# Kernel optimization log

Measured on AMD Instinct MI355X. Metric: run time of the kernel, lower is better.

Reference implementation:

```python
import jax, jax.numpy as jnp
import numpy as np

N = 20000      # num nodes
E = 320000     # num edges (before self loops)
D = 512        # d_model
H = 4          # gnn_heads
C = 256        # gnn_hidden_dim (per-head out channels)
L = 4          # gnn_num_layers
B = 16         # number of graphs in batch
NEG_SLOPE = 0.2
LN_EPS = 1e-5


def setup_inputs() -> dict:
    key = jax.random.key(0)
    ks = jax.random.split(key, 10)
    s = 0.05
    return {
        "x": jax.random.normal(ks[0], (N, D), jnp.float32),
        "edge_index": jax.random.randint(ks[1], (2, E), 0, N, dtype=jnp.int32),
        "batch": jnp.sort(jax.random.randint(ks[2], (N,), 0, B, dtype=jnp.int32)),
        "W0": jax.random.normal(ks[3], (D, H * C), jnp.float32) * s,
        "W_rest": jax.random.normal(ks[4], (L - 1, H * C, H * C), jnp.float32) * s,
        "att_src": jax.random.normal(ks[5], (L, H, C), jnp.float32) * s,
        "att_dst": jax.random.normal(ks[6], (L, H, C), jnp.float32) * s,
        "conv_bias": jnp.zeros((L, H * C), jnp.float32),
        "proj_W": jax.random.normal(ks[7], (H * C, D), jnp.float32) * s,
        "proj_b": jnp.zeros((D,), jnp.float32),
        "ln_gamma": jnp.ones((D,), jnp.float32),
        "ln_beta": jnp.zeros((D,), jnp.float32),
    }


def _gat_layer(x, src, dst, W, a_src, a_dst, b):
    # x: [N, F_in] -> h: [N, H, C]
    h = (x @ W).reshape(N, H, C)
    alpha_src = jnp.einsum('nhc,hc->nh', h, a_src)   # [N, H]
    alpha_dst = jnp.einsum('nhc,hc->nh', h, a_dst)   # [N, H]
    e = jax.nn.leaky_relu(alpha_src[src] + alpha_dst[dst], NEG_SLOPE)  # [Etot, H]
    # per-destination softmax (every node has a self loop, so segments nonempty)
    m = jax.ops.segment_max(e, dst, num_segments=N)
    ex = jnp.exp(e - m[dst])
    denom = jax.ops.segment_sum(ex, dst, num_segments=N)
    alpha = ex / (denom[dst] + 1e-16)                # [Etot, H]
    out = jax.ops.segment_sum(alpha[:, :, None] * h[src], dst, num_segments=N)  # [N, H, C]
    return out.reshape(N, H * C) + b


def reference(x, edge_index, batch, W0, W_rest, att_src, att_dst, conv_bias,
              proj_W, proj_b, ln_gamma, ln_beta):
    # add self loops (PyG GATConv default)
    loop = jnp.arange(N, dtype=edge_index.dtype)
    src = jnp.concatenate([edge_index[0], loop])
    dst = jnp.concatenate([edge_index[1], loop])

    h = x
    for l in range(L):
        W = W0 if l == 0 else W_rest[l - 1]
        h = _gat_layer(h, src, dst, W, att_src[l], att_dst[l], conv_bias[l])
        h = jax.nn.relu(h)  # dropout: eval mode -> identity

    # global mean pool over nodes per graph
    sums = jax.ops.segment_sum(h, batch, num_segments=B)           # [B, H*C]
    counts = jax.ops.segment_sum(jnp.ones((N,), h.dtype), batch, num_segments=B)
    pooled = sums / jnp.maximum(counts, 1.0)[:, None]

    out = pooled @ proj_W + proj_b                                 # [B, D]
    mu = out.mean(-1, keepdims=True)
    var = ((out - mu) ** 2).mean(-1, keepdims=True)
    return (out - mu) / jnp.sqrt(var + LN_EPS) * ln_gamma + ln_beta
```

## Files before the change

kernel.cpp:

```cpp
#include <hip/hip_runtime.h>
#include <hip/hip_bf16.h>
#include <hip/hip_fp8.h>
#include <math.h>

#define Nn 20000
#define Ee 320000
#define Dd 512
#define Hh 4
#define Cc 256
#define Ll 4
#define Bb 16
#define HC 1024
#define ETOT (Ee + Nn)
#define NEG_SLOPE 0.2f
#define LN_EPS 1e-5f
#define NBLK ((Nn + 255) / 256)

typedef __attribute__((ext_vector_type(8))) __bf16 bf16x8;
typedef __attribute__((ext_vector_type(4))) __bf16 bf16x4;
typedef __attribute__((ext_vector_type(4))) float f32x4;
typedef __attribute__((ext_vector_type(2))) float f32x2;

__device__ __forceinline__ f32x4 fp8x4_to_f32(unsigned int v) {
#if __has_builtin(__builtin_amdgcn_cvt_pk_f32_fp8)
    f32x2 lo = __builtin_amdgcn_cvt_pk_f32_fp8((int)v, false);
    f32x2 hi = __builtin_amdgcn_cvt_pk_f32_fp8((int)v, true);
    f32x4 r; r[0] = lo[0]; r[1] = lo[1]; r[2] = hi[0]; r[3] = hi[1];
    return r;
#else
    f32x4 r;
    #pragma unroll
    for (int i = 0; i < 4; ++i) {
        __hip_fp8_e4m3 q; q.__x = (v >> (8 * i)) & 0xff;
        r[i] = (float)q;
    }
    return r;
#endif
}

__device__ __forceinline__ unsigned char f32_to_fp8(float f) {
    return __hip_fp8_e4m3(f).__x;
}


__device__ __forceinline__ void decode_edge(const int* ei, int e, int& s, int& d) {
    if (e < Ee) { s = ei[e]; d = ei[Ee + e]; }
    else        { s = e - Ee; d = e - Ee; }
}

__global__ void count_deg_kernel(const int* __restrict__ ei, int* __restrict__ deg) {
    int e = blockIdx.x * blockDim.x + threadIdx.x;
    if (e >= ETOT) return;
    int s, d; decode_edge(ei, e, s, d);
    atomicAdd(&deg[d], 1);
}

__global__ void scan1_kernel(const int* __restrict__ deg, int* __restrict__ tmp,
                             int* __restrict__ bsum) {
    __shared__ int sd[256];
    int tid = threadIdx.x;
    int i = blockIdx.x * 256 + tid;
    sd[tid] = (i < Nn) ? deg[i] : 0;
    __syncthreads();
    for (int off = 1; off < 256; off <<= 1) {
        int t = (tid >= off) ? sd[tid - off] : 0;
        __syncthreads();
        sd[tid] += t;
        __syncthreads();
    }
    if (i < Nn) tmp[i] = sd[tid];
    if (tid == 255) bsum[blockIdx.x] = sd[255];
}

__global__ void scan2_kernel(int* __restrict__ bsum) {
    __shared__ int sd[256];
    int tid = threadIdx.x;
    sd[tid] = (tid < NBLK) ? bsum[tid] : 0;
    __syncthreads();
    for (int off = 1; off < 256; off <<= 1) {
        int t = (tid >= off) ? sd[tid - off] : 0;
        __syncthreads();
        sd[tid] += t;
        __syncthreads();
    }
    if (tid < NBLK) bsum[tid] = sd[tid];
}

__global__ void scan3_kernel(const int* __restrict__ tmp, const int* __restrict__ bsum,
                             const int* __restrict__ deg,
                             int* __restrict__ row_ptr, int* __restrict__ cursor) {
    int i = blockIdx.x * 256 + threadIdx.x;
    if (i >= Nn) return;
    int boff = (blockIdx.x == 0) ? 0 : bsum[blockIdx.x - 1];
    int incl = tmp[i] + boff;
    row_ptr[i + 1] = incl;
    cursor[i] = incl - deg[i];
    if (i == 0) row_ptr[0] = 0;
}

__global__ void scatter_kernel(const int* __restrict__ ei, int* __restrict__ cursor,
                               int* __restrict__ csr_src) {
    int e = blockIdx.x * blockDim.x + threadIdx.x;
    if (e >= ETOT) return;
    int s, d; decode_edge(ei, e, s, d);
    int pos = atomicAdd(&cursor[d], 1);
    csr_src[pos] = s;
}


__global__ void cast_kernel(const float* __restrict__ in, __bf16* __restrict__ out, int n4) {
    int i = blockIdx.x * blockDim.x + threadIdx.x;
    if (i >= n4) return;
    f32x4 v = ((const f32x4*)in)[i];
    bf16x4 o;
    #pragma unroll
    for (int k = 0; k < 4; ++k) o[k] = (__bf16)v[k];
    ((bf16x4*)out)[i] = o;
}

__global__ void transpose_cast_kernel(const float* __restrict__ W, __bf16* __restrict__ WT,
                                      int K, int N) {
    __shared__ float tile[32][33];
    W  += (size_t)blockIdx.z * K * N;
    WT += (size_t)blockIdx.z * K * N;
    int n0 = blockIdx.x * 32, k0 = blockIdx.y * 32;
    for (int i = threadIdx.y; i < 32; i += 8)
        tile[i][threadIdx.x] = W[(size_t)(k0 + i) * N + n0 + threadIdx.x];
    __syncthreads();
    for (int i = threadIdx.y; i < 32; i += 8)
        WT[(size_t)(n0 + i) * K + k0 + threadIdx.x] = (__bf16)tile[threadIdx.x][i];
}


__device__ __forceinline__ void async16(const __bf16* g, __bf16* l) {
    __builtin_amdgcn_global_load_lds((const __attribute__((address_space(1))) void*)g,
                                     (__attribute__((address_space(3))) void*)l,
                                     16, 0, 0);
}

__global__ __launch_bounds__(256) void mfma_gemm_kernel(
    const __bf16* __restrict__ A,
    const __bf16* __restrict__ BT,
    unsigned char* __restrict__ C8,
    const float* __restrict__ att_s,
    const float* __restrict__ att_d,
    float* __restrict__ aprt_s,
    float* __restrict__ aprt_d,
    int M, int K)
{
    int lin = blockIdx.y * 8 + blockIdx.x;
    int rblk = (lin >> 6) * 8 + (lin & 7);
    int cblk = (lin >> 3) & 7;
    int rowBase = rblk * 128, colBase = cblk * 128;
    if (rowBase >= M) return;

    __shared__ __bf16 As[2][128 * 32];
    __shared__ __bf16 Bs[2][128 * 32];
    int tid = threadIdx.x;
    int wave = tid >> 6, lane = tid & 63;
    int m16 = lane & 15, quad = lane >> 4;
    int waveRow = (wave >> 1) * 64, waveCol = (wave & 1) * 64;

    f32x4 acc[4][4] = {};

    int srow = wave * 32 + (lane >> 2);
    int gch0 = (lane & 3) ^ ((srow >> 1) & 3);
    int gch1 = (lane & 3) ^ (((srow + 16) >> 1) & 3);
    int gr0 = rowBase + srow;       if (gr0 >= M) gr0 = M - 1;
    int gr1 = rowBase + srow + 16;  if (gr1 >= M) gr1 = M - 1;
    int ldsOff = srow * 32 + (lane & 3) * 8;

    for (int k0 = 0; k0 < K; k0 += 64) {
        #pragma unroll
        for (int p = 0; p < 2; ++p) {
            int kp = k0 + p * 32;
            async16(A + (size_t)gr0 * K + kp + gch0 * 8, &As[p][ldsOff]);
            async16(A + (size_t)gr1 * K + kp + gch1 * 8, &As[p][ldsOff + 16 * 32]);
            async16(BT + (size_t)(colBase + srow) * K + kp + gch0 * 8, &Bs[p][ldsOff]);
            async16(BT + (size_t)(colBase + srow + 16) * K + kp + gch1 * 8, &Bs[p][ldsOff + 16 * 32]);
        }
        __syncthreads();
        #pragma unroll
        for (int p = 0; p < 2; ++p) {
            bf16x8 af[4], bfr[4];
            #pragma unroll
            for (int i = 0; i < 4; ++i) {
                int row = waveRow + i * 16 + m16;
                af[i] = *(const bf16x8*)&As[p][row * 32 + (quad ^ ((row >> 1) & 3)) * 8];
                int col = waveCol + i * 16 + m16;
                bfr[i] = *(const bf16x8*)&Bs[p][col * 32 + (quad ^ ((col >> 1) & 3)) * 8];
            }
            #pragma unroll
            for (int i = 0; i < 4; ++i)
                #pragma unroll
                for (int j = 0; j < 4; ++j)
                    acc[i][j] = __builtin_amdgcn_mfma_f32_16x16x32_bf16(af[i], bfr[j], acc[i][j], 0, 0, 0);
        }
        __syncthreads();
    }

    int cbase = colBase + waveCol;
    int head = cbase >> 8;
    int part = (cblk & 1) * 2 + (wave & 1);
    float as4[4], ad4[4];
    #pragma unroll
    for (int j = 0; j < 4; ++j) {
        int off = (cbase + j * 16 + m16) & 255;
        as4[j] = att_s[head * 256 + off];
        ad4[j] = att_d[head * 256 + off];
    }

    #pragma unroll
    for (int i = 0; i < 4; ++i) {
        int r0 = rowBase + waveRow + i * 16 + quad * 4;
        #pragma unroll
        for (int r = 0; r < 4; ++r) {
            int row = r0 + r;
            float ps = 0.f, pd = 0.f;
            #pragma unroll
            for (int j = 0; j < 4; ++j) {
                float h = acc[i][j][r];
                ps += h * as4[j];
                pd += h * ad4[j];
                if (row < M)
                    C8[(size_t)row * HC + colBase + waveCol + j * 16 + m16] = f32_to_fp8(h);
            }
            #pragma unroll
            for (int off = 1; off < 16; off <<= 1) {
                ps += __shfl_xor(ps, off);
                pd += __shfl_xor(pd, off);
            }
            if (m16 == 0 && row < M) {
                aprt_s[((size_t)part * M + row) * 4 + head] = ps;
                aprt_d[((size_t)part * M + row) * 4 + head] = pd;
            }
        }
    }
}


__global__ void alpha_sum_kernel(const float* __restrict__ aprt_s,
                                 const float* __restrict__ aprt_d,
                                 float* __restrict__ asrc, float* __restrict__ adst) {
    int n = blockIdx.x * 256 + threadIdx.x;
    if (n >= Nn) return;
    f32x4 s = {0.f, 0.f, 0.f, 0.f}, d = {0.f, 0.f, 0.f, 0.f};
    #pragma unroll
    for (int p = 0; p < 4; ++p) {
        f32x4 vs = ((const f32x4*)aprt_s)[(size_t)p * Nn + n];
        f32x4 vd = ((const f32x4*)aprt_d)[(size_t)p * Nn + n];
        #pragma unroll
        for (int k = 0; k < 4; ++k) { s[k] += vs[k]; d[k] += vd[k]; }
    }
    ((f32x4*)asrc)[n] = s;
    ((f32x4*)adst)[n] = d;
}


__global__ __launch_bounds__(256) void ew_kernel(const float* __restrict__ asrc,
                                                 const float* __restrict__ adst,
                                                 const int* __restrict__ row_ptr,
                                                 const int* __restrict__ csr_src,
                                                 float* __restrict__ ewT,
                                                 float* __restrict__ dinv) {
    int w = threadIdx.x >> 6, lane = threadIdx.x & 63;
    int n = blockIdx.x * 4 + w;
    if (n >= Nn) return;
    int start = row_ptr[n], end = row_ptr[n + 1];
    f32x4 ad = ((const f32x4*)adst)[n];
    f32x4 d = {0.f, 0.f, 0.f, 0.f};
    for (int e = start + lane; e < end; e += 64) {
        int s = csr_src[e];
        f32x4 as = ((const f32x4*)asrc)[s];
        #pragma unroll
        for (int k = 0; k < 4; ++k) {
            float z = as[k] + ad[k];
            z = (z > 0.f) ? z : NEG_SLOPE * z;
            float ex = __expf(z);
            ewT[(size_t)k * ETOT + e] = ex;
            d[k] += ex;
        }
    }
    #pragma unroll
    for (int off = 32; off > 0; off >>= 1) {
        #pragma unroll
        for (int k = 0; k < 4; ++k) d[k] += __shfl_down(d[k], off);
    }
    if (lane == 0) {
        f32x4 iv;
        #pragma unroll
        for (int k = 0; k < 4; ++k) iv[k] = 1.f / (d[k] + 1e-16f);
        ((f32x4*)dinv)[n] = iv;
    }
}


__global__ __launch_bounds__(256) void agg_slice_kernel(
    const unsigned char* __restrict__ h8,
    const float* __restrict__ ewT,
    const float* __restrict__ dinv,
    const int* __restrict__ row_ptr,
    const int* __restrict__ csr_src,
    const float* __restrict__ bias_l,
    __bf16* __restrict__ outb)
{
    int slice = blockIdx.x;
    int head = slice >> 1;
    int tid = threadIdx.x;
    int nslot = tid >> 4;
    int ch = tid & 15;
    int n = blockIdx.y * 16 + nslot;

    __shared__ int   csr_sh[512];
    __shared__ float ew_sh[512];
    __shared__ int   rp_sh[17];

    if (tid < 17) rp_sh[tid] = row_ptr[blockIdx.y * 16 + tid];
    __syncthreads();
    int blk_lo = rp_sh[0], blk_hi = rp_sh[16];
    int start = rp_sh[nslot], end = rp_sh[nslot + 1];

    const unsigned char* hs = h8 + slice * 128 + ch * 8;
    const float* ewh = ewT + (size_t)head * ETOT;
    float acc[8] = {};

    for (int c0 = blk_lo; c0 < blk_hi; c0 += 512) {
        int c1 = min(c0 + 512, blk_hi);
        int cnt = c1 - c0;
        for (int i = tid; i < cnt; i += 256) {
            csr_sh[i] = csr_src[c0 + i];
            ew_sh[i]  = ewh[c0 + i];
        }
        __syncthreads();
        int lo = max(start, c0), hi = min(end, c1);
        int e = lo;
        for (; e + 1 < hi; e += 2) {
            int s0 = csr_sh[e - c0], s1 = csr_sh[e + 1 - c0];
            float w0 = ew_sh[e - c0], w1 = ew_sh[e + 1 - c0];
            uint2 u0 = *(const uint2*)(hs + (size_t)s0 * HC);
            uint2 u1 = *(const uint2*)(hs + (size_t)s1 * HC);
            f32x4 a0 = fp8x4_to_f32(u0.x), b0 = fp8x4_to_f32(u0.y);
            f32x4 a1 = fp8x4_to_f32(u1.x), b1 = fp8x4_to_f32(u1.y);
            #pragma unroll
            for (int k = 0; k < 4; ++k) {
                acc[k]     += w0 * a0[k];
                acc[k + 4] += w0 * b0[k];
                acc[k]     += w1 * a1[k];
                acc[k + 4] += w1 * b1[k];
            }
        }
        if (e < hi) {
            int s0 = csr_sh[e - c0];
            float w0 = ew_sh[e - c0];
            uint2 u0 = *(const uint2*)(hs + (size_t)s0 * HC);
            f32x4 a0 = fp8x4_to_f32(u0.x), b0 = fp8x4_to_f32(u0.y);
            #pragma unroll
            for (int k = 0; k < 4; ++k) {
                acc[k]     += w0 * a0[k];
                acc[k + 4] += w0 * b0[k];
            }
        }
        __syncthreads();
    }

    float inv = dinv[n * 4 + head];
    bf16x8 o;
    #pragma unroll
    for (int k = 0; k < 8; ++k)
        o[k] = (__bf16)fmaxf(acc[k] * inv + bias_l[slice * 128 + ch * 8 + k], 0.f);
    *(bf16x8*)(outb + (size_t)n * HC + slice * 128 + ch * 8) = o;
}


__device__ __forceinline__ int lower_bound_batch(const int* __restrict__ batch, int val) {
    int lo = 0, hi = Nn;
    while (lo < hi) { int mid = (lo + hi) >> 1; if (batch[mid] < val) lo = mid + 1; else hi = mid; }
    return lo;
}

__global__ void pool_kernel(const __bf16* __restrict__ h2b, const int* __restrict__ batch,
                            float* __restrict__ pooledP) {
    int b = blockIdx.x, part = blockIdx.y;
    int tid = threadIdx.x;
    int start = lower_bound_batch(batch, b);
    int end   = lower_bound_batch(batch, b + 1);
    int len = end - start;
    int chunk = (len + 7) / 8;
    int s0 = start + part * chunk;
    int s1 = min(s0 + chunk, end);
    float acc[4] = {0.f, 0.f, 0.f, 0.f};
    for (int n = s0; n < s1; ++n) {
        bf16x4 v = ((const bf16x4*)(h2b + (size_t)n * HC))[tid];
        #pragma unroll
        for (int k = 0; k < 4; ++k) acc[k] += (float)v[k];
    }
    #pragma unroll
    for (int k = 0; k < 4; ++k)
        pooledP[((size_t)part * Bb + b) * HC + tid * 4 + k] = acc[k];
}


__global__ __launch_bounds__(512) void proj_partial_kernel(const float* __restrict__ pooledP,
                                                           const int* __restrict__ batch,
                                                           const float* __restrict__ projW,
                                                           float* __restrict__ projP) {
    int b = blockIdx.x, part = blockIdx.y;
    int d = threadIdx.x;
    __shared__ float psum[HC];
    int start = lower_bound_batch(batch, b);
    int end   = lower_bound_batch(batch, b + 1);
    float inv = 1.0f / fmaxf((float)(end - start), 1.0f);
    for (int k = d; k < HC; k += 512) {
        float s = 0.f;
        #pragma unroll
        for (int p = 0; p < 8; ++p) s += pooledP[((size_t)p * Bb + b) * HC + k];
        psum[k] = s * inv;
    }
    __syncthreads();
    float acc = 0.f;
    int k0 = part * 128;
    for (int k = k0; k < k0 + 128; ++k)
        acc += psum[k] * projW[(size_t)k * Dd + d];
    projP[((size_t)part * Bb + b) * Dd + d] = acc;
}

__global__ __launch_bounds__(512) void ln_kernel(const float* __restrict__ projP,
                                                 const float* __restrict__ projb,
                                                 const float* __restrict__ gamma,
                                                 const float* __restrict__ beta,
                                                 float* __restrict__ out) {
    int b = blockIdx.x;
    int d = threadIdx.x;
    __shared__ float red[512];
    float o = projb[d];
    #pragma unroll
    for (int p = 0; p < 8; ++p) o += projP[((size_t)p * Bb + b) * Dd + d];
    red[d] = o;
    __syncthreads();
    for (int off = 256; off > 0; off >>= 1) {
        if (d < off) red[d] += red[d + off];
        __syncthreads();
    }
    float mu = red[0] / (float)Dd;
    __syncthreads();
    float df = o - mu;
    red[d] = df * df;
    __syncthreads();
    for (int off = 256; off > 0; off >>= 1) {
        if (d < off) red[d] += red[d + off];
        __syncthreads();
    }
    float var = red[0] / (float)Dd;
    out[b * Dd + d] = df / sqrtf(var + LN_EPS) * gamma[d] + beta[d];
}


extern "C" void kernel_launch(void* const* d_in, const int* in_sizes, int n_in,
                              void* d_out, int out_size, void* d_ws, size_t ws_size,
                              hipStream_t stream) {
    const float* x         = (const float*)d_in[0];
    const int*   ei        = (const int*)d_in[1];
    const int*   batch     = (const int*)d_in[2];
    const float* W0        = (const float*)d_in[3];
    const float* W_rest    = (const float*)d_in[4];
    const float* att_src   = (const float*)d_in[5];
    const float* att_dst   = (const float*)d_in[6];
    const float* conv_bias = (const float*)d_in[7];
    const float* proj_W    = (const float*)d_in[8];
    const float* proj_b    = (const float*)d_in[9];
    const float* ln_gamma  = (const float*)d_in[10];
    const float* ln_beta   = (const float*)d_in[11];
    float* out = (float*)d_out;

    char* ws = (char*)d_ws;
    size_t off = 0;
    auto alloc = [&](size_t bytes) {
        void* p = ws + off;
        off = (off + bytes + 255) & ~(size_t)255;
        return p;
    };
    unsigned char* h8 = (unsigned char*)alloc((size_t)Nn * HC);
    __bf16* h2b     = (__bf16*)alloc((size_t)Nn * HC * 2);
    __bf16* xb      = (__bf16*)alloc((size_t)Nn * Dd * 2);
    __bf16* W0T     = (__bf16*)alloc((size_t)HC * Dd * 2);
    __bf16* WrT     = (__bf16*)alloc((size_t)3 * HC * HC * 2);
    float*  aprt_s  = (float*)alloc((size_t)4 * Nn * Hh * 4);
    float*  aprt_d  = (float*)alloc((size_t)4 * Nn * Hh * 4);
    float*  asrc    = (float*)alloc((size_t)Nn * Hh * 4);
    float*  adst    = (float*)alloc((size_t)Nn * Hh * 4);
    float*  ewT     = (float*)alloc((size_t)Hh * ETOT * 4);
    float*  dinv    = (float*)alloc((size_t)Nn * Hh * 4);
    int*    deg     = (int*)alloc((size_t)Nn * 4);
    int*    tmp     = (int*)alloc((size_t)Nn * 4);
    int*    bsum    = (int*)alloc((size_t)256 * 4);
    int*    row_ptr = (int*)alloc((size_t)(Nn + 1) * 4);
    int*    cursor  = (int*)alloc((size_t)Nn * 4);
    int*    csr_src = (int*)alloc((size_t)ETOT * 4);
    float*  pooledP = (float*)alloc((size_t)8 * Bb * HC * 4);
    float*  projP   = (float*)alloc((size_t)8 * Bb * Dd * 4);
    (void)ws_size; (void)in_sizes; (void)n_in; (void)out_size;

    hipMemsetAsync(deg, 0, (size_t)Nn * 4, stream);
    count_deg_kernel<<<(ETOT + 255) / 256, 256, 0, stream>>>(ei, deg);
    scan1_kernel<<<NBLK, 256, 0, stream>>>(deg, tmp, bsum);
    scan2_kernel<<<1, 256, 0, stream>>>(bsum);
    scan3_kernel<<<NBLK, 256, 0, stream>>>(tmp, bsum, deg, row_ptr, cursor);
    scatter_kernel<<<(ETOT + 255) / 256, 256, 0, stream>>>(ei, cursor, csr_src);

    cast_kernel<<<(Nn * Dd / 4 + 255) / 256, 256, 0, stream>>>(x, xb, Nn * Dd / 4);
    transpose_cast_kernel<<<dim3(HC / 32, Dd / 32, 1), dim3(32, 8), 0, stream>>>(W0, W0T, Dd, HC);
    transpose_cast_kernel<<<dim3(HC / 32, HC / 32, 3), dim3(32, 8), 0, stream>>>(W_rest, WrT, HC, HC);

    dim3 gemm_grid(8, 160);
    for (int l = 0; l < Ll; ++l) {
        const __bf16* Afeat = (l == 0) ? xb : h2b;
        int K = (l == 0) ? Dd : HC;
        const __bf16* BT = (l == 0) ? W0T : (WrT + (size_t)(l - 1) * HC * HC);
        mfma_gemm_kernel<<<gemm_grid, 256, 0, stream>>>(
            Afeat, BT, h8, att_src + l * HC, att_dst + l * HC, aprt_s, aprt_d, Nn, K);
        alpha_sum_kernel<<<NBLK, 256, 0, stream>>>(aprt_s, aprt_d, asrc, adst);
        ew_kernel<<<(Nn + 3) / 4, 256, 0, stream>>>(asrc, adst, row_ptr, csr_src, ewT, dinv);
        agg_slice_kernel<<<dim3(8, Nn / 16), 256, 0, stream>>>(
            h8, ewT, dinv, row_ptr, csr_src, conv_bias + l * HC, h2b);
    }

    pool_kernel<<<dim3(Bb, 8), 256, 0, stream>>>(h2b, batch, pooledP);
    proj_partial_kernel<<<dim3(Bb, 8), 512, 0, stream>>>(pooledP, batch, proj_W, projP);
    ln_kernel<<<Bb, 512, 0, stream>>>(projP, proj_b, ln_gamma, ln_beta, out);
}
```

Before: 650.3 us.

## Double-buffer GEMM with 128x256 tiles, 512 threads and prefetch overlap

The GEMM moves from 128x128 tiles with 4 waves to 128x256 tiles with 8 waves, doubling the LDS buffers. The next k-tile is staged asynchronously while the MFMAs on the current one run, using explicit vmcnt waits, raw barriers and setprio around the MFMA block. The goal is to hide global-load latency and raise B-tile reuse. In exchange, LDS use per block rises to 96KB, which lowers occupancy, and the hand-tuned waitcnt logic is fragile.

```diff
diff --git a/kernel.cpp b/kernel.cpp
--- a/kernel.cpp
+++ b/kernel.cpp
@@ -138,7 +138,39 @@
                                      16, 0, 0);
 }
 
-__global__ __launch_bounds__(256) void mfma_gemm_kernel(
+#define GEMM_PHASE(BUF, KP, DO_STAGE, KT_NEXT, VM_LAST)                                   \
+  {                                                                                       \
+    bf16x8 af[4], bv[4];                                                                  \
+    _Pragma("unroll")                                                                     \
+    for (int i = 0; i < 4; ++i) {                                                         \
+        int row = waveRow + i * 16 + m16;                                                 \
+        af[i] = *(const bf16x8*)&As[BUF][KP][row * 32 + ((quad ^ ((row >> 1) & 3)) << 3)];\
+        int col = waveCol + i * 16 + m16;                                                 \
+        bv[i] = *(const bf16x8*)&Bs[BUF][KP][col * 32 + ((quad ^ ((col >> 1) & 3)) << 3)];\
+    }                                                                                     \
+    if (DO_STAGE) {                                                                       \
+        int kk = (KT_NEXT) * 64 + (KP) * 32;                                              \
+        async16(A  + (size_t)gra  * K + kk + (gca << 3), &As[(BUF) ^ 1][KP][ldsA]);       \
+        async16(BT + (size_t)grb  * K + kk + (gcb << 3), &Bs[(BUF) ^ 1][KP][ldsB]);       \
+        async16(BT + (size_t)grb2 * K + kk + (gcb << 3), &Bs[(BUF) ^ 1][KP][ldsB2]);      \
+    }                                                                                     \
+    if (VM_LAST) { asm volatile("s_waitcnt vmcnt(0)" ::: "memory"); }                     \
+    else         { asm volatile("s_waitcnt vmcnt(3)" ::: "memory"); }                     \
+    __builtin_amdgcn_s_barrier();                                                         \
+    asm volatile("s_waitcnt lgkmcnt(0)" ::: "memory");                                    \
+    __builtin_amdgcn_sched_barrier(0);                                                    \
+    __builtin_amdgcn_s_setprio(1);                                                        \
+    _Pragma("unroll")                                                                     \
+    for (int i = 0; i < 4; ++i)                                                           \
+        _Pragma("unroll")                                                                 \
+        for (int j = 0; j < 4; ++j)                                                       \
+            acc[i][j] = __builtin_amdgcn_mfma_f32_16x16x32_bf16(af[i], bv[j],             \
+                                                                acc[i][j], 0, 0, 0);      \
+    __builtin_amdgcn_s_setprio(0);                                                        \
+    __builtin_amdgcn_s_barrier();                                                         \
+  }
+
+__global__ __launch_bounds__(512) void mfma_gemm_kernel(
     const __bf16* __restrict__ A,
     const __bf16* __restrict__ BT,
     unsigned char* __restrict__ C8,
@@ -148,60 +180,54 @@
     float* __restrict__ aprt_d,
     int M, int K)
 {
-    int lin = blockIdx.y * 8 + blockIdx.x;
-    int rblk = (lin >> 6) * 8 + (lin & 7);
-    int cblk = (lin >> 3) & 7;
-    int rowBase = rblk * 128, colBase = cblk * 128;
+    int lin = blockIdx.y * 4 + blockIdx.x;
+    int rblk = (lin >> 5) * 8 + (lin & 7);
+    int cblk = (lin >> 3) & 3;
+    int rowBase = rblk * 128, colBase = cblk * 256;
     if (rowBase >= M) return;
 
-    __shared__ __bf16 As[2][128 * 32];
-    __shared__ __bf16 Bs[2][128 * 32];
+    __shared__ __bf16 As[2][2][128 * 32];
+    __shared__ __bf16 Bs[2][2][256 * 32];
     int tid = threadIdx.x;
     int wave = tid >> 6, lane = tid & 63;
     int m16 = lane & 15, quad = lane >> 4;
-    int waveRow = (wave >> 1) * 64, waveCol = (wave & 1) * 64;
+    int wm = wave >> 2, wn = wave & 3;
+    int waveRow = wm * 64, waveCol = wn * 64;
 
     f32x4 acc[4][4] = {};
 
-    int srow = wave * 32 + (lane >> 2);
-    int gch0 = (lane & 3) ^ ((srow >> 1) & 3);
-    int gch1 = (lane & 3) ^ (((srow + 16) >> 1) & 3);
-    int gr0 = rowBase + srow;       if (gr0 >= M) gr0 = M - 1;
-    int gr1 = rowBase + srow + 16;  if (gr1 >= M) gr1 = M - 1;
-    int ldsOff = srow * 32 + (lane & 3) * 8;
-
-    for (int k0 = 0; k0 < K; k0 += 64) {
-        #pragma unroll
-        for (int p = 0; p < 2; ++p) {
-            int kp = k0 + p * 32;
-            async16(A + (size_t)gr0 * K + kp + gch0 * 8, &As[p][ldsOff]);
-            async16(A + (size_t)gr1 * K + kp + gch1 * 8, &As[p][ldsOff + 16 * 32]);
-            async16(BT + (size_t)(colBase + srow) * K + kp + gch0 * 8, &Bs[p][ldsOff]);
-            async16(BT + (size_t)(colBase + srow + 16) * K + kp + gch1 * 8, &Bs[p][ldsOff + 16 * 32]);
-        }
-        __syncthreads();
-        #pragma unroll
-        for (int p = 0; p < 2; ++p) {
-            bf16x8 af[4], bfr[4];
-            #pragma unroll
-            for (int i = 0; i < 4; ++i) {
-                int row = waveRow + i * 16 + m16;
-                af[i] = *(const bf16x8*)&As[p][row * 32 + (quad ^ ((row >> 1) & 3)) * 8];
-                int col = waveCol + i * 16 + m16;
-                bfr[i] = *(const bf16x8*)&Bs[p][col * 32 + (quad ^ ((col >> 1) & 3)) * 8];
-            }
-            #pragma unroll
-            for (int i = 0; i < 4; ++i)
-                #pragma unroll
-                for (int j = 0; j < 4; ++j)
-                    acc[i][j] = __builtin_amdgcn_mfma_f32_16x16x32_bf16(af[i], bfr[j], acc[i][j], 0, 0, 0);
-        }
-        __syncthreads();
+    int srow = tid >> 2;
+    int chk  = tid & 3;
+    int gca  = chk ^ ((srow >> 1) & 3);
+    int gcb  = gca;
+    int gra  = rowBase + srow;  if (gra >= M) gra = M - 1;
+    int grb  = colBase + srow;
+    int grb2 = colBase + srow + 128;
+    int ldsA  = srow * 32 + chk * 8;
+    int ldsB  = srow * 32 + chk * 8;
+    int ldsB2 = ldsB + 128 * 32;
+
+    #pragma unroll
+    for (int kp = 0; kp < 2; ++kp) {
+        int kk = kp * 32;
+        async16(A  + (size_t)gra  * K + kk + (gca << 3), &As[0][kp][ldsA]);
+        async16(BT + (size_t)grb  * K + kk + (gcb << 3), &Bs[0][kp][ldsB]);
+        async16(BT + (size_t)grb2 * K + kk + (gcb << 3), &Bs[0][kp][ldsB2]);
+    }
+    asm volatile("s_waitcnt vmcnt(3)" ::: "memory");
+    __builtin_amdgcn_s_barrier();
+
+    int NT = K >> 6;
+    for (int kt = 0; kt < NT; ++kt) {
+        int buf = kt & 1;
+        bool more = (kt + 1 < NT);
+        GEMM_PHASE(buf, 0, more, kt + 1, !more);
+        GEMM_PHASE(buf, 1, more, kt + 1, false);
     }
 
     int cbase = colBase + waveCol;
     int head = cbase >> 8;
-    int part = (cblk & 1) * 2 + (wave & 1);
+    int part = wn;
     float as4[4], ad4[4];
     #pragma unroll
     for (int j = 0; j < 4; ++j) {
@@ -223,12 +249,12 @@
                 ps += h * as4[j];
                 pd += h * ad4[j];
                 if (row < M)
-                    C8[(size_t)row * HC + colBase + waveCol + j * 16 + m16] = f32_to_fp8(h);
+                    C8[(size_t)row * HC + cbase + j * 16 + m16] = f32_to_fp8(h);
             }
             #pragma unroll
-            for (int off = 1; off < 16; off <<= 1) {
-                ps += __shfl_xor(ps, off);
-                pd += __shfl_xor(pd, off);
+            for (int off2 = 1; off2 < 16; off2 <<= 1) {
+                ps += __shfl_xor(ps, off2);
+                pd += __shfl_xor(pd, off2);
             }
             if (m16 == 0 && row < M) {
                 aprt_s[((size_t)part * M + row) * 4 + head] = ps;
@@ -511,12 +537,12 @@
     transpose_cast_kernel<<<dim3(HC / 32, Dd / 32, 1), dim3(32, 8), 0, stream>>>(W0, W0T, Dd, HC);
     transpose_cast_kernel<<<dim3(HC / 32, HC / 32, 3), dim3(32, 8), 0, stream>>>(W_rest, WrT, HC, HC);
 
-    dim3 gemm_grid(8, 160);
+    dim3 gemm_grid(4, 160);
     for (int l = 0; l < Ll; ++l) {
         const __bf16* Afeat = (l == 0) ? xb : h2b;
         int K = (l == 0) ? Dd : HC;
         const __bf16* BT = (l == 0) ? W0T : (WrT + (size_t)(l - 1) * HC * HC);
-        mfma_gemm_kernel<<<gemm_grid, 256, 0, stream>>>(
+        mfma_gemm_kernel<<<gemm_grid, 512, 0, stream>>>(
             Afeat, BT, h8, att_src + l * HC, att_dst + l * HC, aprt_s, aprt_d, Nn, K);
         alpha_sum_kernel<<<NBLK, 256, 0, stream>>>(aprt_s, aprt_d, asrc, adst);
         ew_kernel<<<(Nn + 3) / 4, 256, 0, stream>>>(asrc, adst, row_ptr, csr_src, ewT, dinv);
```

Measured after the change: 722.0 us. 1.11x slower.

## Narrow per-node thread groups in edge-weight and aggregation kernels

Applied to the files above, without the earlier changes.

The edge-weight kernel now gives each node 16 lanes instead of a full 64-lane wavefront, since the average degree is about 17, and reduces with xor shuffles. The aggregation kernel now covers 32 nodes per block with 8 threads per node, each loading 16 fp8 bytes per gathered row instead of 8. Edge source and weight are packed into one int2 shared array with a larger staging chunk, and the 2-way edge unroll is dropped. The goal is fewer idle lanes and fewer, wider gather loads, at the cost of more registers per thread and less unrolling for memory-level parallelism.

```diff
diff --git a/kernel.cpp b/kernel.cpp
--- a/kernel.cpp
+++ b/kernel.cpp
@@ -263,13 +263,13 @@
                                                  const int* __restrict__ csr_src,
                                                  float* __restrict__ ewT,
                                                  float* __restrict__ dinv) {
-    int w = threadIdx.x >> 6, lane = threadIdx.x & 63;
-    int n = blockIdx.x * 4 + w;
+    int grp = threadIdx.x >> 4, lane16 = threadIdx.x & 15;
+    int n = blockIdx.x * 16 + grp;
     if (n >= Nn) return;
     int start = row_ptr[n], end = row_ptr[n + 1];
     f32x4 ad = ((const f32x4*)adst)[n];
     f32x4 d = {0.f, 0.f, 0.f, 0.f};
-    for (int e = start + lane; e < end; e += 64) {
+    for (int e = start + lane16; e < end; e += 16) {
         int s = csr_src[e];
         f32x4 as = ((const f32x4*)asrc)[s];
         #pragma unroll
@@ -282,11 +282,11 @@
         }
     }
     #pragma unroll
-    for (int off = 32; off > 0; off >>= 1) {
-        #pragma unroll
-        for (int k = 0; k < 4; ++k) d[k] += __shfl_down(d[k], off);
-    }
-    if (lane == 0) {
+    for (int off = 8; off > 0; off >>= 1) {
+        #pragma unroll
+        for (int k = 0; k < 4; ++k) d[k] += __shfl_xor(d[k], off);
+    }
+    if (lane16 == 0) {
         f32x4 iv;
         #pragma unroll
         for (int k = 0; k < 4; ++k) iv[k] = 1.f / (d[k] + 1e-16f);
@@ -307,68 +307,59 @@
     int slice = blockIdx.x;
     int head = slice >> 1;
     int tid = threadIdx.x;
-    int nslot = tid >> 4;
-    int ch = tid & 15;
-    int n = blockIdx.y * 16 + nslot;
-
-    __shared__ int   csr_sh[512];
-    __shared__ float ew_sh[512];
-    __shared__ int   rp_sh[17];
-
-    if (tid < 17) rp_sh[tid] = row_ptr[blockIdx.y * 16 + tid];
-    __syncthreads();
-    int blk_lo = rp_sh[0], blk_hi = rp_sh[16];
+    int nslot = tid >> 3;
+    int ch = tid & 7;
+    int n = blockIdx.y * 32 + nslot;
+
+    __shared__ int2 ce_sh[1024];
+    __shared__ int  rp_sh[33];
+
+    if (tid < 33) rp_sh[tid] = row_ptr[blockIdx.y * 32 + tid];
+    __syncthreads();
+    int blk_lo = rp_sh[0], blk_hi = rp_sh[32];
     int start = rp_sh[nslot], end = rp_sh[nslot + 1];
 
-    const unsigned char* hs = h8 + slice * 128 + ch * 8;
+    const unsigned char* hs = h8 + slice * 128 + ch * 16;
     const float* ewh = ewT + (size_t)head * ETOT;
-    float acc[8] = {};
-
-    for (int c0 = blk_lo; c0 < blk_hi; c0 += 512) {
-        int c1 = min(c0 + 512, blk_hi);
+    float acc[16] = {};
+
+    for (int c0 = blk_lo; c0 < blk_hi; c0 += 1024) {
+        int c1 = min(c0 + 1024, blk_hi);
         int cnt = c1 - c0;
         for (int i = tid; i < cnt; i += 256) {
-            csr_sh[i] = csr_src[c0 + i];
-            ew_sh[i]  = ewh[c0 + i];
+            int2 v;
+            v.x = csr_src[c0 + i];
+            v.y = __float_as_int(ewh[c0 + i]);
+            ce_sh[i] = v;
         }
         __syncthreads();
         int lo = max(start, c0), hi = min(end, c1);
-        int e = lo;
-        for (; e + 1 < hi; e += 2) {
-            int s0 = csr_sh[e - c0], s1 = csr_sh[e + 1 - c0];
-            float w0 = ew_sh[e - c0], w1 = ew_sh[e + 1 - c0];
-            uint2 u0 = *(const uint2*)(hs + (size_t)s0 * HC);
-            uint2 u1 = *(const uint2*)(hs + (size_t)s1 * HC);
-            f32x4 a0 = fp8x4_to_f32(u0.x), b0 = fp8x4_to_f32(u0.y);
-            f32x4 a1 = fp8x4_to_f32(u1.x), b1 = fp8x4_to_f32(u1.y);
+        for (int e = lo; e < hi; ++e) {
+            int2 v = ce_sh[e - c0];
+            float w = __int_as_float(v.y);
+            uint4 u = *(const uint4*)(hs + (size_t)v.x * HC);
+            f32x4 a0 = fp8x4_to_f32(u.x), a1 = fp8x4_to_f32(u.y);
+            f32x4 a2 = fp8x4_to_f32(u.z), a3 = fp8x4_to_f32(u.w);
             #pragma unroll
             for (int k = 0; k < 4; ++k) {
-                acc[k]     += w0 * a0[k];
-                acc[k + 4] += w0 * b0[k];
-                acc[k]     += w1 * a1[k];
-                acc[k + 4] += w1 * b1[k];
+                acc[k]      += w * a0[k];
+                acc[k + 4]  += w * a1[k];
+                acc[k + 8]  += w * a2[k];
+                acc[k + 12] += w * a3[k];
             }
         }
-        if (e < hi) {
-            int s0 = csr_sh[e - c0];
-            float w0 = ew_sh[e - c0];
-            uint2 u0 = *(const uint2*)(hs + (size_t)s0 * HC);
-            f32x4 a0 = fp8x4_to_f32(u0.x), b0 = fp8x4_to_f32(u0.y);
-            #pragma unroll
-            for (int k = 0; k < 4; ++k) {
-                acc[k]     += w0 * a0[k];
-                acc[k + 4] += w0 * b0[k];
-            }
-        }
         __syncthreads();
     }
 
     float inv = dinv[n * 4 + head];
-    bf16x8 o;
-    #pragma unroll
-    for (int k = 0; k < 8; ++k)
-        o[k] = (__bf16)fmaxf(acc[k] * inv + bias_l[slice * 128 + ch * 8 + k], 0.f);
-    *(bf16x8*)(outb + (size_t)n * HC + slice * 128 + ch * 8) = o;
+    bf16x8 o0, o1;
+    #pragma unroll
+    for (int k = 0; k < 8; ++k) {
+        o0[k] = (__bf16)fmaxf(acc[k] * inv + bias_l[slice * 128 + ch * 16 + k], 0.f);
+        o1[k] = (__bf16)fmaxf(acc[k + 8] * inv + bias_l[slice * 128 + ch * 16 + 8 + k], 0.f);
+    }
+    *(bf16x8*)(outb + (size_t)n * HC + slice * 128 + ch * 16) = o0;
+    *(bf16x8*)(outb + (size_t)n * HC + slice * 128 + ch * 16 + 8) = o1;
 }
 
 
@@ -519,8 +510,8 @@
         mfma_gemm_kernel<<<gemm_grid, 256, 0, stream>>>(
             Afeat, BT, h8, att_src + l * HC, att_dst + l * HC, aprt_s, aprt_d, Nn, K);
         alpha_sum_kernel<<<NBLK, 256, 0, stream>>>(aprt_s, aprt_d, asrc, adst);
-        ew_kernel<<<(Nn + 3) / 4, 256, 0, stream>>>(asrc, adst, row_ptr, csr_src, ewT, dinv);
-        agg_slice_kernel<<<dim3(8, Nn / 16), 256, 0, stream>>>(
+        ew_kernel<<<(Nn + 15) / 16, 256, 0, stream>>>(asrc, adst, row_ptr, csr_src, ewT, dinv);
+        agg_slice_kernel<<<dim3(8, Nn / 32), 256, 0, stream>>>(
             h8, ewT, dinv, row_ptr, csr_src, conv_bias + l * HC, h2b);
     }
 
```

After: 629.2 us. -3.2%, faster.
